# Optimization experiments

Hardware: AMD Instinct MI355X
Metric: run time of the kernel (lower is better)

## Reference

```python
import jax, jax.numpy as jnp
import numpy as np

N, IN, H, C = 50000, 128, 4, 32
E = 800000
NEG_SLOPE = 0.2


def setup_inputs() -> dict:
    key = jax.random.key(0)
    ks = jax.random.split(key, 8)
    x = jax.random.normal(ks[0], (N, IN), dtype=jnp.float32)
    edge_index = jax.random.randint(ks[1], (2, E), 0, N, dtype=jnp.int64)
    s = 0.1
    W = jax.random.normal(ks[2], (H * C, IN), dtype=jnp.float32) * s
    att_src = jax.random.normal(ks[3], (1, H, C), dtype=jnp.float32) * s
    att_dst = jax.random.normal(ks[4], (1, H, C), dtype=jnp.float32) * s
    bias = jnp.zeros((H * C,), dtype=jnp.float32)
    skip_W = jax.random.normal(ks[5], (H * C, IN), dtype=jnp.float32) * s
    skip_b = jnp.zeros((H * C,), dtype=jnp.float32)
    return {"x": x, "edge_index": edge_index, "W": W, "att_src": att_src,
            "att_dst": att_dst, "bias": bias, "skip_W": skip_W, "skip_b": skip_b}


def reference(x, edge_index, W, att_src, att_dst, bias, skip_W, skip_b):
    src, dst = edge_index[0], edge_index[1]
    # projected node features: [N, H, C]
    xp = (x @ W.T).reshape(N, H, C)
    # per-node attention logits: [N, H]
    a_src = jnp.sum(xp * att_src, axis=-1)
    a_dst = jnp.sum(xp * att_dst, axis=-1)
    # edge logits with LeakyReLU: [E, H]
    e = a_src[src] + a_dst[dst]
    e = jnp.where(e > 0, e, NEG_SLOPE * e)
    # segment softmax over incoming edges of each dst node
    m = jax.ops.segment_max(e, dst, num_segments=N)  # [N, H]
    ex = jnp.exp(e - m[dst])
    denom = jax.ops.segment_sum(ex, dst, num_segments=N)  # [N, H]
    alpha = ex / (denom[dst] + 1e-16)
    # weighted messages and scatter-add aggregation: [N, H, C]
    msg = alpha[:, :, None] * xp[src]
    agg = jax.ops.segment_sum(msg, dst, num_segments=N)
    x_gat = agg.reshape(N, H * C) + bias
    x_skip = x @ skip_W.T + skip_b
    return jax.nn.elu(x_gat + x_skip)
```

## Files before the change

### kernel.cpp

```cpp
#include <hip/hip_runtime.h>
#include <hip/hip_bf16.h>


#define NN 50000
#define EE 800000
#define FD 128
#define NEG_SLOPE 0.2f

#define SCB 1024
#define NB_SC ((NN + SCB - 1) / SCB)
#define NB_PRE 782
#define NB_CONVW 32
#define NB_MFMA (NN / 16)
#define NB_FILL 782

typedef __attribute__((ext_vector_type(8))) short short8;
typedef __attribute__((ext_vector_type(4))) float f32x4;

__device__ inline ushort f2b(float f) {
    __hip_bfloat16 h = __float2bfloat16(f);
    return *reinterpret_cast<ushort*>(&h);
}
__device__ inline float b2f(ushort u) {
    union { float f; unsigned int i; } c;
    c.i = ((unsigned int)u) << 16;
    return c.f;
}

__global__ __launch_bounds__(256) void gat_pre_kernel(
    const int* __restrict__ idx, int* __restrict__ count, int* __restrict__ rank,
    const float* __restrict__ W, const float* __restrict__ skip_W,
    ushort* __restrict__ wb)
{
    int b = blockIdx.x;
    if (b < NB_PRE) {
        int base = (b * 256 + threadIdx.x) * 4;
        if (base >= EE) return;
        int4 dd = *reinterpret_cast<const int4*>(idx + EE + base);
        int4 rr;
        rr.x = atomicAdd(&count[dd.x], 1);
        rr.y = atomicAdd(&count[dd.y], 1);
        rr.z = atomicAdd(&count[dd.z], 1);
        rr.w = atomicAdd(&count[dd.w], 1);
        *reinterpret_cast<int4*>(rank + base) = rr;
    } else {
        int i = ((b - NB_PRE) * 256 + threadIdx.x) * 4;
        int row = i >> 7;
        int colb = i & 127;
        const float* src = (row < 128) ? (W + row * FD + colb)
                                       : (skip_W + (row - 128) * FD + colb);
        float4 v = *reinterpret_cast<const float4*>(src);
        ushort4 o;
        o.x = f2b(v.x); o.y = f2b(v.y); o.z = f2b(v.z); o.w = f2b(v.w);
        *reinterpret_cast<ushort4*>(wb + i) = o;
    }
}

__global__ __launch_bounds__(1024) void gat_scan_kernel(
    const int* __restrict__ count, int* __restrict__ rowptr)
{
    __shared__ int ws[16];
    __shared__ int boff_s;
    int tid = threadIdx.x, lane = tid & 63, wv = tid >> 6;

    int ps = 0;
    for (int i = tid; i < blockIdx.x * SCB; i += SCB) ps += count[i];
    #pragma unroll
    for (int off = 32; off; off >>= 1) ps += __shfl_down(ps, off, 64);
    if (lane == 0) ws[wv] = ps;
    __syncthreads();
    if (wv == 0) {
        int t = (lane < 16) ? ws[lane] : 0;
        #pragma unroll
        for (int off = 8; off; off >>= 1) t += __shfl_down(t, off, 64);
        if (lane == 0) boff_s = t;
    }
    __syncthreads();

    int i = blockIdx.x * SCB + tid;
    int v = (i < NN) ? count[i] : 0;
    int incl = v;
    #pragma unroll
    for (int off = 1; off < 64; off <<= 1) {
        int t = __shfl_up(incl, off, 64);
        if (lane >= off) incl += t;
    }
    if (lane == 63) ws[wv] = incl;
    __syncthreads();
    if (wv == 0) {
        int t = (lane < 16) ? ws[lane] : 0;
        int winc = t;
        #pragma unroll
        for (int off = 1; off < 16; off <<= 1) {
            int u = __shfl_up(winc, off, 64);
            if (lane >= off) winc += u;
        }
        if (lane < 16) ws[lane] = winc - t;
    }
    __syncthreads();
    int excl = boff_s + ws[wv] + incl - v;
    if (i < NN) rowptr[i] = excl;
    if (blockIdx.x == 0 && tid == 0) rowptr[NN] = EE;
}

__global__ __launch_bounds__(256) void gat_mfma_fill_kernel(
    const float* __restrict__ x, const ushort* __restrict__ wb,
    const float* __restrict__ att_src, const float* __restrict__ att_dst,
    const float* __restrict__ bias, const float* __restrict__ skip_b,
    ushort* __restrict__ xpb, float* __restrict__ a_src, float* __restrict__ a_dst,
    float* __restrict__ skip,
    const int* __restrict__ idx, const int* __restrict__ rank,
    const int* __restrict__ rowptr, int* __restrict__ col)
{
    if (blockIdx.x >= NB_MFMA) {
        int base = ((blockIdx.x - NB_MFMA) * 256 + threadIdx.x) * 4;
        if (base + 4 > EE) return;
        int4 dd = *reinterpret_cast<const int4*>(idx + EE + base);
        int4 rr = *reinterpret_cast<const int4*>(rank + base);
        int4 ss = *reinterpret_cast<const int4*>(idx + base);
        int p0 = rowptr[dd.x] + rr.x;
        int p1 = rowptr[dd.y] + rr.y;
        int p2 = rowptr[dd.z] + rr.z;
        int p3 = rowptr[dd.w] + rr.w;
        col[p0] = ss.x;
        col[p1] = ss.y;
        col[p2] = ss.z;
        col[p3] = ss.w;
        return;
    }

    const int p = blockIdx.x;
    const int tid = threadIdx.x;
    const int w = tid >> 6;
    const int l = tid & 63;
    const int lrow = l & 15;
    const int lgrp = l >> 4;
    const int m0 = p * 16;
    const int is_skip = w >> 1;
    const int ncb = (w & 1) * 64;

    short8 bfrag[4][4];
    const ushort* wbase = wb + (size_t)(is_skip * 128 + ncb) * FD;
    #pragma unroll
    for (int t = 0; t < 4; ++t)
        #pragma unroll
        for (int kk = 0; kk < 4; ++kk)
            bfrag[t][kk] = *reinterpret_cast<const short8*>(
                wbase + (size_t)(t * 16 + lrow) * FD + kk * 32 + lgrp * 8);

    short8 afrag[4];
    const float* xrow = x + (size_t)(m0 + lrow) * FD + lgrp * 8;
    #pragma unroll
    for (int kk = 0; kk < 4; ++kk) {
        float4 a0 = *reinterpret_cast<const float4*>(xrow + kk * 32);
        float4 a1 = *reinterpret_cast<const float4*>(xrow + kk * 32 + 4);
        short8 af;
        af[0] = f2b(a0.x); af[1] = f2b(a0.y); af[2] = f2b(a0.z); af[3] = f2b(a0.w);
        af[4] = f2b(a1.x); af[5] = f2b(a1.y); af[6] = f2b(a1.z); af[7] = f2b(a1.w);
        afrag[kk] = af;
    }

    f32x4 acc[4];
    #pragma unroll
    for (int t = 0; t < 4; ++t) acc[t] = (f32x4){0.f, 0.f, 0.f, 0.f};

    #pragma unroll
    for (int kk = 0; kk < 4; ++kk)
        #pragma unroll
        for (int t = 0; t < 4; ++t)
            acc[t] = __builtin_amdgcn_mfma_f32_16x16x32_bf16(
                afrag[kk], bfrag[t][kk], acc[t], 0, 0, 0);

    if (is_skip) {
        #pragma unroll
        for (int t = 0; t < 4; ++t) {
            int colt = ncb + t * 16 + lrow;
            float add = skip_b[colt] + bias[colt];
            #pragma unroll
            for (int r = 0; r < 4; ++r) {
                int row = m0 + lgrp * 4 + r;
                skip[(size_t)row * FD + colt] = acc[t][r] + add;
            }
        }
    } else {
        float as[4], ad[4];
        #pragma unroll
        for (int t = 0; t < 4; ++t) {
            int colt = ncb + t * 16 + lrow;
            as[t] = att_src[colt];
            ad[t] = att_dst[colt];
            #pragma unroll
            for (int r = 0; r < 4; ++r) {
                int row = m0 + lgrp * 4 + r;
                xpb[(size_t)row * FD + colt] = f2b(acc[t][r]);
            }
        }
        const int h0 = ncb >> 5;
        #pragma unroll
        for (int r = 0; r < 4; ++r) {
            float p0 = acc[0][r] * as[0] + acc[1][r] * as[1];
            float p1 = acc[2][r] * as[2] + acc[3][r] * as[3];
            float q0 = acc[0][r] * ad[0] + acc[1][r] * ad[1];
            float q1 = acc[2][r] * ad[2] + acc[3][r] * ad[3];
            #pragma unroll
            for (int m = 1; m < 16; m <<= 1) {
                p0 += __shfl_xor(p0, m, 64);
                p1 += __shfl_xor(p1, m, 64);
                q0 += __shfl_xor(q0, m, 64);
                q1 += __shfl_xor(q1, m, 64);
            }
            if (lrow == 0) {
                int row = m0 + lgrp * 4 + r;
                a_src[(size_t)row * 4 + h0]     = p0;
                a_src[(size_t)row * 4 + h0 + 1] = p1;
                a_dst[(size_t)row * 4 + h0]     = q0;
                a_dst[(size_t)row * 4 + h0 + 1] = q1;
            }
        }
    }
}

__global__ __launch_bounds__(256) void gat_gather_kernel(
    const int* __restrict__ rowptr, const int* __restrict__ col,
    const float* __restrict__ a_src, const float* __restrict__ a_dst,
    const ushort* __restrict__ xpb, const float* __restrict__ skip,
    float* __restrict__ out)
{
    int wid = (blockIdx.x * 256 + threadIdx.x) >> 6;
    const int d = __builtin_amdgcn_readfirstlane(wid);
    int lane = threadIdx.x & 63;
    const int h = lane >> 4;
    const int ch = lane * 2;
    const float ad = a_dst[(size_t)d * 4 + h];
    const int beg = rowptr[d], end = rowptr[d + 1];
    float2 sk = *reinterpret_cast<const float2*>(skip + (size_t)d * FD + ch);

    float accx = 0.f, accy = 0.f, asum = 0.f;
    int j = beg;
    for (; j + 4 <= end; j += 4) {
        int s0 = __builtin_amdgcn_readfirstlane(col[j]);
        int s1 = __builtin_amdgcn_readfirstlane(col[j + 1]);
        int s2 = __builtin_amdgcn_readfirstlane(col[j + 2]);
        int s3 = __builtin_amdgcn_readfirstlane(col[j + 3]);
        float e0 = a_src[(size_t)s0 * 4 + h] + ad;
        float e1 = a_src[(size_t)s1 * 4 + h] + ad;
        float e2 = a_src[(size_t)s2 * 4 + h] + ad;
        float e3 = a_src[(size_t)s3 * 4 + h] + ad;
        ushort2 x0 = *reinterpret_cast<const ushort2*>(xpb + (size_t)s0 * FD + ch);
        ushort2 x1 = *reinterpret_cast<const ushort2*>(xpb + (size_t)s1 * FD + ch);
        ushort2 x2 = *reinterpret_cast<const ushort2*>(xpb + (size_t)s2 * FD + ch);
        ushort2 x3 = *reinterpret_cast<const ushort2*>(xpb + (size_t)s3 * FD + ch);
        e0 = e0 > 0.f ? e0 : NEG_SLOPE * e0;
        e1 = e1 > 0.f ? e1 : NEG_SLOPE * e1;
        e2 = e2 > 0.f ? e2 : NEG_SLOPE * e2;
        e3 = e3 > 0.f ? e3 : NEG_SLOPE * e3;
        float p0 = __expf(e0), p1 = __expf(e1), p2 = __expf(e2), p3 = __expf(e3);
        asum += (p0 + p1) + (p2 + p3);
        accx += p0 * b2f(x0.x) + p1 * b2f(x1.x) + p2 * b2f(x2.x) + p3 * b2f(x3.x);
        accy += p0 * b2f(x0.y) + p1 * b2f(x1.y) + p2 * b2f(x2.y) + p3 * b2f(x3.y);
    }
    for (; j < end; ++j) {
        int s = __builtin_amdgcn_readfirstlane(col[j]);
        float e = a_src[(size_t)s * 4 + h] + ad;
        ushort2 xv = *reinterpret_cast<const ushort2*>(xpb + (size_t)s * FD + ch);
        e = e > 0.f ? e : NEG_SLOPE * e;
        float pe = __expf(e);
        asum += pe;
        accx += pe * b2f(xv.x);
        accy += pe * b2f(xv.y);
    }
    float inv = 1.f / (asum + 1e-16f);
    float r0 = sk.x + accx * inv;
    float r1 = sk.y + accy * inv;
    r0 = r0 > 0.f ? r0 : expm1f(r0);
    r1 = r1 > 0.f ? r1 : expm1f(r1);
    *reinterpret_cast<float2*>(out + (size_t)d * FD + ch) = make_float2(r0, r1);
}

extern "C" void kernel_launch(void* const* d_in, const int* in_sizes, int n_in,
                              void* d_out, int out_size, void* d_ws, size_t ws_size,
                              hipStream_t stream)
{
    const float* x       = (const float*)d_in[0];
    const int*   idx     = (const int*)d_in[1];
    const float* W       = (const float*)d_in[2];
    const float* att_src = (const float*)d_in[3];
    const float* att_dst = (const float*)d_in[4];
    const float* bias    = (const float*)d_in[5];
    const float* skip_W  = (const float*)d_in[6];
    const float* skip_b  = (const float*)d_in[7];
    float*       out     = (float*)d_out;

    float*  ws     = (float*)d_ws;
    float*  skip   = ws;
    float*  a_src  = ws + 6400000;
    float*  a_dst  = ws + 6600000;
    int*    count  = (int*)(ws + 6800000);
    int*    rowptr = (int*)(ws + 6852000);
    int*    col    = (int*)(ws + 6956000);
    int*    rank   = (int*)(ws + 7756000);
    ushort* xpb    = (ushort*)(ws + 8600000);
    ushort* wb     = (ushort*)(ws + 11900000);

    hipMemsetAsync(count, 0, (size_t)NN * sizeof(int), stream);

    gat_pre_kernel<<<NB_PRE + NB_CONVW, 256, 0, stream>>>(idx, count, rank, W, skip_W, wb);

    gat_scan_kernel<<<NB_SC, SCB, 0, stream>>>(count, rowptr);

    gat_mfma_fill_kernel<<<NB_MFMA + NB_FILL, 256, 0, stream>>>(
        x, wb, att_src, att_dst, bias, skip_b, xpb, a_src, a_dst, skip,
        idx, rank, rowptr, col);

    gat_gather_kernel<<<(NN * 64) / 256, 256, 0, stream>>>(
        rowptr, col, a_src, a_dst, xpb, skip, out);
}
```

Before: 142.2 us.

## Split each node's edge range across two wavefronts and reorder fill blocks first

The gather kernel now gives each destination node two wavefronts. Each one covers half of the incoming edges, and the partial sums and softmax denominators are combined through shared memory. The fill/MFMA kernel puts the edge-fill blocks before the MFMA blocks so the scatter work starts first. This aims to shorten per-wave serial latency and improve latency hiding in the gather. The cost is twice as many waves, an extra block sync, and dropping readfirstlane on col indices, which may make those loads vector rather than scalar.

```diff
diff --git a/kernel.cpp b/kernel.cpp
--- a/kernel.cpp
+++ b/kernel.cpp
@@ -11,8 +11,8 @@
 #define NB_SC ((NN + SCB - 1) / SCB)
 #define NB_PRE 782
 #define NB_CONVW 32
+#define NB_FILL 782
 #define NB_MFMA (NN / 16)
-#define NB_FILL 782
 
 typedef __attribute__((ext_vector_type(8))) short short8;
 typedef __attribute__((ext_vector_type(4))) float f32x4;
@@ -103,7 +103,7 @@
     if (blockIdx.x == 0 && tid == 0) rowptr[NN] = EE;
 }
 
-__global__ __launch_bounds__(256) void gat_mfma_fill_kernel(
+__global__ __launch_bounds__(256) void gat_fill_mfma_kernel(
     const float* __restrict__ x, const ushort* __restrict__ wb,
     const float* __restrict__ att_src, const float* __restrict__ att_dst,
     const float* __restrict__ bias, const float* __restrict__ skip_b,
@@ -112,8 +112,8 @@
     const int* __restrict__ idx, const int* __restrict__ rank,
     const int* __restrict__ rowptr, int* __restrict__ col)
 {
-    if (blockIdx.x >= NB_MFMA) {
-        int base = ((blockIdx.x - NB_MFMA) * 256 + threadIdx.x) * 4;
+    if (blockIdx.x < NB_FILL) {
+        int base = (blockIdx.x * 256 + threadIdx.x) * 4;
         if (base + 4 > EE) return;
         int4 dd = *reinterpret_cast<const int4*>(idx + EE + base);
         int4 rr = *reinterpret_cast<const int4*>(rank + base);
@@ -129,7 +129,7 @@
         return;
     }
 
-    const int p = blockIdx.x;
+    const int p = blockIdx.x - NB_FILL;
     const int tid = threadIdx.x;
     const int w = tid >> 6;
     const int l = tid & 63;
@@ -226,22 +226,24 @@
     const ushort* __restrict__ xpb, const float* __restrict__ skip,
     float* __restrict__ out)
 {
-    int wid = (blockIdx.x * 256 + threadIdx.x) >> 6;
-    const int d = __builtin_amdgcn_readfirstlane(wid);
-    int lane = threadIdx.x & 63;
+    __shared__ float lpart[4][64][3];
+    const int lw = threadIdx.x >> 6;
+    const int lane = threadIdx.x & 63;
+    const int gw = blockIdx.x * 4 + lw;
+    const int d = gw >> 1;
+    const int half = gw & 1;
     const int h = lane >> 4;
     const int ch = lane * 2;
     const float ad = a_dst[(size_t)d * 4 + h];
-    const int beg = rowptr[d], end = rowptr[d + 1];
-    float2 sk = *reinterpret_cast<const float2*>(skip + (size_t)d * FD + ch);
+    const int beg0 = rowptr[d], end0 = rowptr[d + 1];
+    const int mid = beg0 + ((end0 - beg0 + 1) >> 1);
+    const int beg = half ? mid : beg0;
+    const int end = half ? end0 : mid;
 
     float accx = 0.f, accy = 0.f, asum = 0.f;
     int j = beg;
     for (; j + 4 <= end; j += 4) {
-        int s0 = __builtin_amdgcn_readfirstlane(col[j]);
-        int s1 = __builtin_amdgcn_readfirstlane(col[j + 1]);
-        int s2 = __builtin_amdgcn_readfirstlane(col[j + 2]);
-        int s3 = __builtin_amdgcn_readfirstlane(col[j + 3]);
+        int s0 = col[j], s1 = col[j + 1], s2 = col[j + 2], s3 = col[j + 3];
         float e0 = a_src[(size_t)s0 * 4 + h] + ad;
         float e1 = a_src[(size_t)s1 * 4 + h] + ad;
         float e2 = a_src[(size_t)s2 * 4 + h] + ad;
@@ -260,7 +262,7 @@
         accy += p0 * b2f(x0.y) + p1 * b2f(x1.y) + p2 * b2f(x2.y) + p3 * b2f(x3.y);
     }
     for (; j < end; ++j) {
-        int s = __builtin_amdgcn_readfirstlane(col[j]);
+        int s = col[j];
         float e = a_src[(size_t)s * 4 + h] + ad;
         ushort2 xv = *reinterpret_cast<const ushort2*>(xpb + (size_t)s * FD + ch);
         e = e > 0.f ? e : NEG_SLOPE * e;
@@ -269,7 +271,20 @@
         accx += pe * b2f(xv.x);
         accy += pe * b2f(xv.y);
     }
+
+    if (half) {
+        lpart[lw][lane][0] = accx;
+        lpart[lw][lane][1] = accy;
+        lpart[lw][lane][2] = asum;
+    }
+    __syncthreads();
+    if (half) return;
+    accx += lpart[lw ^ 1][lane][0];
+    accy += lpart[lw ^ 1][lane][1];
+    asum += lpart[lw ^ 1][lane][2];
+
     float inv = 1.f / (asum + 1e-16f);
+    float2 sk = *reinterpret_cast<const float2*>(skip + (size_t)d * FD + ch);
     float r0 = sk.x + accx * inv;
     float r1 = sk.y + accy * inv;
     r0 = r0 > 0.f ? r0 : expm1f(r0);
@@ -308,10 +323,10 @@
 
     gat_scan_kernel<<<NB_SC, SCB, 0, stream>>>(count, rowptr);
 
-    gat_mfma_fill_kernel<<<NB_MFMA + NB_FILL, 256, 0, stream>>>(
+    gat_fill_mfma_kernel<<<NB_FILL + NB_MFMA, 256, 0, stream>>>(
         x, wb, att_src, att_dst, bias, skip_b, xpb, a_src, a_dst, skip,
         idx, rank, rowptr, col);
 
-    gat_gather_kernel<<<(NN * 64) / 256, 256, 0, stream>>>(
+    gat_gather_kernel<<<(NN * 2 * 64) / 256, 256, 0, stream>>>(
         rowptr, col, a_src, a_dst, xpb, skip, out);
 }
```

New measurement: 158.2 us. 1.11x slower.

## Partition CSR fill by destination range per block and drop readfirstlane in gather

Applied to the files above, without the earlier changes.

The CSR column fill becomes 256 blocks at the front of the grid. Each block scans the entire edge list and writes only the edges whose destination falls in its own range of 196 nodes, so the col writes from one block land in a contiguous region instead of scattering across the whole array. The cost is that every fill block reads all 800K destination indices, which multiplies idx read traffic by about 256 (mostly L2 hits). The gather loop also drops readfirstlane on the loaded column indices, which lets the compiler decide whether they are uniform.

```diff
diff --git a/kernel.cpp b/kernel.cpp
--- a/kernel.cpp
+++ b/kernel.cpp
@@ -11,8 +11,9 @@
 #define NB_SC ((NN + SCB - 1) / SCB)
 #define NB_PRE 782
 #define NB_CONVW 32
+#define NB_FILLS 256
+#define DPC 196
 #define NB_MFMA (NN / 16)
-#define NB_FILL 782
 
 typedef __attribute__((ext_vector_type(8))) short short8;
 typedef __attribute__((ext_vector_type(4))) float f32x4;
@@ -103,7 +104,7 @@
     if (blockIdx.x == 0 && tid == 0) rowptr[NN] = EE;
 }
 
-__global__ __launch_bounds__(256) void gat_mfma_fill_kernel(
+__global__ __launch_bounds__(256) void gat_fill_mfma_kernel(
     const float* __restrict__ x, const ushort* __restrict__ wb,
     const float* __restrict__ att_src, const float* __restrict__ att_dst,
     const float* __restrict__ bias, const float* __restrict__ skip_b,
@@ -112,24 +113,22 @@
     const int* __restrict__ idx, const int* __restrict__ rank,
     const int* __restrict__ rowptr, int* __restrict__ col)
 {
-    if (blockIdx.x >= NB_MFMA) {
-        int base = ((blockIdx.x - NB_MFMA) * 256 + threadIdx.x) * 4;
-        if (base + 4 > EE) return;
-        int4 dd = *reinterpret_cast<const int4*>(idx + EE + base);
-        int4 rr = *reinterpret_cast<const int4*>(rank + base);
-        int4 ss = *reinterpret_cast<const int4*>(idx + base);
-        int p0 = rowptr[dd.x] + rr.x;
-        int p1 = rowptr[dd.y] + rr.y;
-        int p2 = rowptr[dd.z] + rr.z;
-        int p3 = rowptr[dd.w] + rr.w;
-        col[p0] = ss.x;
-        col[p1] = ss.y;
-        col[p2] = ss.z;
-        col[p3] = ss.w;
+    if (blockIdx.x < NB_FILLS) {
+        const int dlo = blockIdx.x * DPC;
+        const int dhi = dlo + DPC;
+        for (int i = 0; i < (EE + 1023) / 1024; ++i) {
+            int base = (i * 256 + threadIdx.x) * 4;
+            if (base >= EE) break;
+            int4 dd = *reinterpret_cast<const int4*>(idx + EE + base);
+            if (dd.x >= dlo && dd.x < dhi) col[rowptr[dd.x] + rank[base]]     = idx[base];
+            if (dd.y >= dlo && dd.y < dhi) col[rowptr[dd.y] + rank[base + 1]] = idx[base + 1];
+            if (dd.z >= dlo && dd.z < dhi) col[rowptr[dd.z] + rank[base + 2]] = idx[base + 2];
+            if (dd.w >= dlo && dd.w < dhi) col[rowptr[dd.w] + rank[base + 3]] = idx[base + 3];
+        }
         return;
     }
 
-    const int p = blockIdx.x;
+    const int p = blockIdx.x - NB_FILLS;
     const int tid = threadIdx.x;
     const int w = tid >> 6;
     const int l = tid & 63;
@@ -238,10 +237,7 @@
     float accx = 0.f, accy = 0.f, asum = 0.f;
     int j = beg;
     for (; j + 4 <= end; j += 4) {
-        int s0 = __builtin_amdgcn_readfirstlane(col[j]);
-        int s1 = __builtin_amdgcn_readfirstlane(col[j + 1]);
-        int s2 = __builtin_amdgcn_readfirstlane(col[j + 2]);
-        int s3 = __builtin_amdgcn_readfirstlane(col[j + 3]);
+        int s0 = col[j], s1 = col[j + 1], s2 = col[j + 2], s3 = col[j + 3];
         float e0 = a_src[(size_t)s0 * 4 + h] + ad;
         float e1 = a_src[(size_t)s1 * 4 + h] + ad;
         float e2 = a_src[(size_t)s2 * 4 + h] + ad;
@@ -260,7 +256,7 @@
         accy += p0 * b2f(x0.y) + p1 * b2f(x1.y) + p2 * b2f(x2.y) + p3 * b2f(x3.y);
     }
     for (; j < end; ++j) {
-        int s = __builtin_amdgcn_readfirstlane(col[j]);
+        int s = col[j];
         float e = a_src[(size_t)s * 4 + h] + ad;
         ushort2 xv = *reinterpret_cast<const ushort2*>(xpb + (size_t)s * FD + ch);
         e = e > 0.f ? e : NEG_SLOPE * e;
@@ -308,7 +304,7 @@
 
     gat_scan_kernel<<<NB_SC, SCB, 0, stream>>>(count, rowptr);
 
-    gat_mfma_fill_kernel<<<NB_MFMA + NB_FILL, 256, 0, stream>>>(
+    gat_fill_mfma_kernel<<<NB_FILLS + NB_MFMA, 256, 0, stream>>>(
         x, wb, att_src, att_dst, bias, skip_b, xpb, a_src, a_dst, skip,
         idx, rank, rowptr, col);
 
```

Measured after the change: 476.8 us. +235.3%, slower.
